# Performance work log

Measured on AMD Instinct MI355X. Metric: run time of the kernel, lower is better.

## Reference

```python
import jax, jax.numpy as jnp
import numpy as np

ALPHA = 5.0
EPS = 1e-12  # avoids inf grad of sqrt at the self-distance (exact 0)


def setup_inputs() -> dict:
    key = jax.random.key(0)
    xyz = jax.random.normal(key, (4, 8192, 3), dtype=jnp.float32)
    return {"xyz": xyz, "nbr_size": 2}


def reference(xyz, nbr_size):
    # Brute-force KNN of xyz against itself (self is included with dist 0,
    # matching pointops.knn(query, ref) when query == ref).
    sq = jnp.sum(xyz * xyz, axis=-1)                      # (B, N)
    # squared pairwise distances: ||a||^2 + ||b||^2 - 2 a.b  -> (B, N, N)
    d2 = sq[:, :, None] + sq[:, None, :] - 2.0 * jnp.einsum(
        'bnd,bmd->bnm', xyz, xyz)
    neg_top, _idx = jax.lax.top_k(-d2, nbr_size)          # (B, N, k) smallest d2
    dist = jnp.sqrt(jnp.maximum(-neg_top, EPS))           # Euclidean distance
    dsum = dist.sum(-1)                                   # (B, N)
    avg_dist = dsum.mean(-1, keepdims=True)               # (B, 1)
    # loss = sum of per-point distance sums exceeding alpha * mean
    loss = jnp.where(dsum > avg_dist * ALPHA, dsum, 0.0).sum()
    return loss
```

## Files before the change

### kernel.cpp

```cpp
#include <hip/hip_runtime.h>

#define BB 4
#define NN 8192
#define BN (BB * NN)
#define ALPHA 5.0f
#define EPSF 1e-12f
#define BLOCK 256
#define QPT 16
#define QB (BLOCK * QPT)
#define BIGF 1e30f

__global__ __launch_bounds__(BLOCK) void prep_kernel(
    const float* __restrict__ xyz, float4* __restrict__ refs4) {
  int g = blockIdx.x * BLOCK + threadIdx.x;
  float x = xyz[3 * g + 0], y = xyz[3 * g + 1], z = xyz[3 * g + 2];
  float hpp = 0.5f * fmaf(x, x, fmaf(y, y, z * z));
  refs4[g] = make_float4(x, y, z, hpp);
}

template <int NSEG>
__global__ __launch_bounds__(BLOCK) void knn_kernel(
    const float4* __restrict__ refs4, float2* __restrict__ pairs) {
  constexpr int SEG = NN / NSEG;
  constexpr int CHUNKS = NN / QB;
  int bid = blockIdx.x;
  int s = bid % NSEG;
  int rem = bid / NSEG;
  int qchunk = rem % CHUNKS;
  int b = rem / CHUNKS;

  const float4* __restrict__ qb4 = refs4 + (size_t)b * NN;

  __shared__ float4 tile[SEG];
  for (int r0 = threadIdx.x; r0 < SEG; r0 += BLOCK)
    tile[r0] = qb4[s * SEG + r0];

  float nqx[QPT], nqy[QPT], nqz[QPT], hq[QPT], m1[QPT], m2[QPT];
#pragma unroll
  for (int i = 0; i < QPT; i++) {
    int q = qchunk * QB + threadIdx.x + i * BLOCK;
    float4 qp = qb4[q];
    nqx[i] = -qp.x;
    nqy[i] = -qp.y;
    nqz[i] = -qp.z;
    hq[i] = qp.w;
    m1[i] = BIGF;
    m2[i] = BIGF;
  }
  __syncthreads();

#pragma unroll 2
  for (int j = 0; j < SEG; j++) {
    float4 p = tile[j];
#pragma unroll
    for (int i = 0; i < QPT; i++) {
      float t = fmaf(nqx[i], p.x, p.w);
      t = fmaf(nqy[i], p.y, t);
      t = fmaf(nqz[i], p.z, t);
      m2[i] = __builtin_amdgcn_fmed3f(t, m1[i], m2[i]);
      m1[i] = fminf(m1[i], t);
    }
  }

#pragma unroll
  for (int i = 0; i < QPT; i++) {
    int q = qchunk * QB + threadIdx.x + i * BLOCK;
    pairs[(size_t)s * BN + b * NN + q] =
        make_float2(m1[i] + hq[i], m2[i] + hq[i]);
  }
}

#define MBLK 128
#define NPART (BN / MBLK)
template <int NSEG>
__global__ __launch_bounds__(MBLK) void merge_kernel(
    const float2* __restrict__ pairs, float* __restrict__ dsum,
    float* __restrict__ partial) {
  int g = blockIdx.x * MBLK + threadIdx.x;
  float m1 = BIGF, m2 = BIGF;
#pragma unroll 8
  for (int s = 0; s < NSEG; s++) {
    float2 p = pairs[(size_t)s * BN + g];
    float n2 = __builtin_amdgcn_fmed3f(p.x, m1, m2);
    m1 = fminf(m1, p.x);
    m2 = n2;
    n2 = __builtin_amdgcn_fmed3f(p.y, m1, m2);
    m1 = fminf(m1, p.y);
    m2 = n2;
  }
  float ds = sqrtf(fmaxf(m1 + m1, EPSF)) + sqrtf(fmaxf(m2 + m2, EPSF));
  dsum[g] = ds;

  float v = ds;
#pragma unroll
  for (int off = 32; off > 0; off >>= 1) v += __shfl_down(v, off, 64);
  __shared__ float warp_sums[MBLK / 64];
  if ((threadIdx.x & 63) == 0) warp_sums[threadIdx.x >> 6] = v;
  __syncthreads();
  if (threadIdx.x == 0) {
    float t = 0.0f;
#pragma unroll
    for (int w = 0; w < MBLK / 64; w++) t += warp_sums[w];
    partial[blockIdx.x] = t;
  }
}

#define LBLK 1024
__global__ __launch_bounds__(LBLK) void loss_kernel(
    const float* __restrict__ dsum, const float* __restrict__ partial,
    float* __restrict__ out) {
  __shared__ float s_avg[BB];
  if (threadIdx.x < NPART) {
    float v = partial[threadIdx.x];
#pragma unroll
    for (int off = 32; off > 0; off >>= 1) v += __shfl_down(v, off, 64);
    if ((threadIdx.x & 63) == 0) s_avg[threadIdx.x >> 6] = v * (ALPHA / NN);
  }
  __syncthreads();

  const float4* d4 = (const float4*)dsum;
  float acc = 0.0f;
#pragma unroll
  for (int it = 0; it < BN / (LBLK * 4); it++) {
    int idx = it * LBLK + threadIdx.x;
    float4 v = d4[idx];
    float thr = s_avg[idx >> 11];
    acc += (v.x > thr) ? v.x : 0.0f;
    acc += (v.y > thr) ? v.y : 0.0f;
    acc += (v.z > thr) ? v.z : 0.0f;
    acc += (v.w > thr) ? v.w : 0.0f;
  }
#pragma unroll
  for (int off = 32; off > 0; off >>= 1) acc += __shfl_down(acc, off, 64);
  __shared__ float warp_sums[LBLK / 64];
  if ((threadIdx.x & 63) == 0) warp_sums[threadIdx.x >> 6] = acc;
  __syncthreads();
  if (threadIdx.x == 0) {
    float t = 0.0f;
#pragma unroll
    for (int w = 0; w < LBLK / 64; w++) t += warp_sums[w];
    out[0] = t;
  }
}

template <int NSEG>
static void run(const float* xyz, float* out, void* d_ws, hipStream_t stream) {
  float2* pairs = (float2*)d_ws;
  float4* refs4 = (float4*)(pairs + (size_t)NSEG * BN);
  float* dsum = (float*)(refs4 + BN);
  float* partial = dsum + BN;
  prep_kernel<<<BN / BLOCK, BLOCK, 0, stream>>>(xyz, refs4);
  int grid1 = BB * (NN / QB) * NSEG;
  knn_kernel<NSEG><<<grid1, BLOCK, 0, stream>>>(refs4, pairs);
  merge_kernel<NSEG><<<BN / MBLK, MBLK, 0, stream>>>(pairs, dsum, partial);
  loss_kernel<<<1, LBLK, 0, stream>>>(dsum, partial, out);
}

extern "C" void kernel_launch(void* const* d_in, const int* in_sizes, int n_in,
                              void* d_out, int out_size, void* d_ws,
                              size_t ws_size, hipStream_t stream) {
  const float* xyz = (const float*)d_in[0];
  float* out = (float*)d_out;

  auto need = [](int nseg) {
    return (size_t)nseg * BN * sizeof(float2) + BN * sizeof(float4) +
           BN * sizeof(float) + NPART * sizeof(float);
  };
  if (ws_size >= need(64)) {
    run<64>(xyz, out, d_ws, stream);
  } else if (ws_size >= need(32)) {
    run<32>(xyz, out, d_ws, stream);
  } else {
    run<16>(xyz, out, d_ws, stream);
  }
}
```

Measured before the change: 105.8 us.

## Halve queries per thread, use SoA shared tile and recompute ref norms

Reduces queries per thread from 16 to 8 and sets a minimum of 4 blocks per SM via launch bounds, doubling the grid to raise occupancy. The shared reference tile becomes three SoA arrays read with 4-wide vector loads. The half-norm of each reference point is now recomputed in the inner loop instead of being read from shared memory. This trades extra ALU work and lower per-thread reuse for more waves in flight and fewer LDS instructions.

```diff
diff --git a/kernel.cpp b/kernel.cpp
--- a/kernel.cpp
+++ b/kernel.cpp
@@ -6,7 +6,7 @@
 #define ALPHA 5.0f
 #define EPSF 1e-12f
 #define BLOCK 256
-#define QPT 16
+#define QPT 8
 #define QB (BLOCK * QPT)
 #define BIGF 1e30f
 
@@ -19,7 +19,7 @@
 }
 
 template <int NSEG>
-__global__ __launch_bounds__(BLOCK) void knn_kernel(
+__global__ __launch_bounds__(BLOCK, 4) void knn_kernel(
     const float4* __restrict__ refs4, float2* __restrict__ pairs) {
   constexpr int SEG = NN / NSEG;
   constexpr int CHUNKS = NN / QB;
@@ -31,9 +31,13 @@
 
   const float4* __restrict__ qb4 = refs4 + (size_t)b * NN;
 
-  __shared__ float4 tile[SEG];
-  for (int r0 = threadIdx.x; r0 < SEG; r0 += BLOCK)
-    tile[r0] = qb4[s * SEG + r0];
+  __shared__ float sx[SEG], sy[SEG], sz[SEG];
+  for (int r = threadIdx.x; r < SEG; r += BLOCK) {
+    float4 v = qb4[s * SEG + r];
+    sx[r] = v.x;
+    sy[r] = v.y;
+    sz[r] = v.z;
+  }
 
   float nqx[QPT], nqy[QPT], nqz[QPT], hq[QPT], m1[QPT], m2[QPT];
 #pragma unroll
@@ -49,16 +53,25 @@
   }
   __syncthreads();
 
-#pragma unroll 2
-  for (int j = 0; j < SEG; j++) {
-    float4 p = tile[j];
+#pragma unroll 1
+  for (int j = 0; j < SEG; j += 4) {
+    float4 px = *(const float4*)&sx[j];
+    float4 py = *(const float4*)&sy[j];
+    float4 pz = *(const float4*)&sz[j];
+    float rx[4] = {px.x, px.y, px.z, px.w};
+    float ry[4] = {py.x, py.y, py.z, py.w};
+    float rz[4] = {pz.x, pz.y, pz.z, pz.w};
 #pragma unroll
-    for (int i = 0; i < QPT; i++) {
-      float t = fmaf(nqx[i], p.x, p.w);
-      t = fmaf(nqy[i], p.y, t);
-      t = fmaf(nqz[i], p.z, t);
-      m2[i] = __builtin_amdgcn_fmed3f(t, m1[i], m2[i]);
-      m1[i] = fminf(m1[i], t);
+    for (int k = 0; k < 4; k++) {
+      float w = 0.5f * fmaf(rx[k], rx[k], fmaf(ry[k], ry[k], rz[k] * rz[k]));
+#pragma unroll
+      for (int i = 0; i < QPT; i++) {
+        float t = fmaf(nqx[i], rx[k], w);
+        t = fmaf(nqy[i], ry[k], t);
+        t = fmaf(nqz[i], rz[k], t);
+        m2[i] = __builtin_amdgcn_fmed3f(t, m1[i], m2[i]);
+        m1[i] = fminf(m1[i], t);
+      }
     }
   }
 
```

Result: faster. 102.3 us (-3.3%).
